# Kernel optimization log

Hardware: AMD Instinct MI355X
Metric: run time of the kernel (lower is better)

The kernel has to match this reference:

```python
import jax, jax.numpy as jnp
import numpy as np

D_MODEL = 1024
NUM_HEADS = 16
DEPTH = D_MODEL // NUM_HEADS


def setup_inputs() -> dict:
    key = jax.random.key(0)
    ks = jax.random.split(key, 11)
    B, S, D = 2, 2048, D_MODEL
    s = 1.0 / np.sqrt(D)
    inp = {
        'x': jax.random.normal(ks[0], (B, S, D), jnp.float32),
        'pH': jax.random.normal(ks[1], (B, 1, 1), jnp.float32),
        'Wq': jax.random.normal(ks[2], (D, D), jnp.float32) * s,
        'bq': jnp.zeros((D,), jnp.float32),
        'Wk': jax.random.normal(ks[3], (D, D), jnp.float32) * s,
        'bk': jnp.zeros((D,), jnp.float32),
        'Wv': jax.random.normal(ks[4], (D, D), jnp.float32) * s,
        'bv': jnp.zeros((D,), jnp.float32),
        'Wo': jax.random.normal(ks[5], (D, D), jnp.float32) * s,
        'bo': jnp.zeros((D,), jnp.float32),
    }
    return inp


def reference(x, pH, Wq, bq, Wk, bk, Wv, bv, Wo, bo):
    B, S, D = x.shape
    H, dh = NUM_HEADS, DEPTH
    # QKV projections -> [B, H, S, dh]
    def proj(W, b):
        return (x @ W + b).reshape(B, S, H, dh).transpose(0, 2, 1, 3)
    q = proj(Wq, bq)
    k = proj(Wk, bk)
    v = proj(Wv, bv)
    # scores [B, H, S, S] with additive per-sample pH bias broadcast over heads/positions
    scores = jnp.einsum('bhqd,bhkd->bhqk', q, k) / jnp.sqrt(jnp.asarray(dh, x.dtype))
    scores = scores + pH[:, :, :, None]  # [B,1,1,1] broadcasts to [B,H,S,S]
    attn = jax.nn.softmax(scores, axis=-1)
    out = jnp.einsum('bhqk,bhkd->bhqd', attn, v)  # [B,H,S,dh]
    out = out.transpose(0, 2, 1, 3).reshape(B, S, D)
    return out @ Wo + bo  # dropout p=0.0 -> identity
```

## Files before the change

### kernel.cpp

```cpp
#include <hip/hip_runtime.h>
#include <hip/hip_bf16.h>
#include <math.h>

#define BATCH 2
#define SEQ   2048
#define DMODEL 1024
#define NHEADS 16
#define DHEAD 64
#define MROWS (BATCH*SEQ)

typedef __attribute__((ext_vector_type(8))) short bf16x8;
typedef __attribute__((ext_vector_type(4))) short bf16x4;
typedef __attribute__((ext_vector_type(4))) float f32x4;

__device__ __forceinline__ short f2bf(float f) {
    union { float f; unsigned u; } c; c.f = f;
    unsigned r = (c.u + 0x7fffu + ((c.u >> 16) & 1u)) >> 16;
    return (short)r;
}
__device__ __forceinline__ float truncmask(unsigned u) {
    union { unsigned u; float f; } c; c.u = u & 0xffff0000u;
    return c.f;
}

__device__ __forceinline__ void async_ld16(const void* g, void* l) {
    __builtin_amdgcn_global_load_lds(
        (const __attribute__((address_space(1))) unsigned*)g,
        (__attribute__((address_space(3))) unsigned*)l, 16, 0, 0);
}

__global__ __launch_bounds__(256) void convert_h(
    const float* __restrict__ in, short* __restrict__ hi, int n8)
{
    const int i = blockIdx.x * 256 + threadIdx.x;
    if (i >= n8) return;
    const float4* p = (const float4*)in + (size_t)i * 2;
    float4 a = p[0], b = p[1];
    float v[8] = {a.x, a.y, a.z, a.w, b.x, b.y, b.z, b.w};
    bf16x8 H;
    #pragma unroll
    for (int j = 0; j < 8; ++j) H[j] = f2bf(v[j]);
    *((bf16x8*)hi + i) = H;
}

__global__ __launch_bounds__(256) void transpose_w4(
    const float* __restrict__ W0, const float* __restrict__ W1,
    const float* __restrict__ W2, const float* __restrict__ W3,
    short* __restrict__ oqkv, short* __restrict__ oo)
{
    __shared__ float T[64][65];
    const int tid = threadIdx.x;
    const int z = blockIdx.z;
    const float* W = (z == 0) ? W0 : (z == 1) ? W1 : (z == 2) ? W2 : W3;
    short* out = (z < 3) ? (oqkv + (size_t)z * 1024 * 1024) : oo;
    const int n0 = blockIdx.x * 64, k0 = blockIdx.y * 64;
    #pragma unroll
    for (int i = 0; i < 16; ++i) {
        const int idx = tid + i * 256;
        const int r = idx >> 6, c = idx & 63;
        T[r][c] = W[(size_t)(k0 + r) * DMODEL + n0 + c];
    }
    __syncthreads();
    #pragma unroll
    for (int i = 0; i < 4; ++i) {
        const int idx = tid + i * 256;
        const int r = idx >> 4, g = idx & 15;
        bf16x4 H;
        #pragma unroll
        for (int j = 0; j < 4; ++j)
            H[j] = f2bf(T[g * 4 + j][r]);
        *(bf16x4*)(out + (size_t)(n0 + r) * DMODEL + k0 + g * 4) = H;
    }
}

#define GBK 64

__global__ __launch_bounds__(256) void mfma_gemm(
    const short* __restrict__ Ahi, const short* __restrict__ Bthi,
    const float* __restrict__ b0, const float* __restrict__ b1, const float* __restrict__ b2,
    short* __restrict__ oqh, short* __restrict__ okh, short* __restrict__ ovh,
    float* __restrict__ outf, int mode, float qscale)
{
    __shared__ short Ah[128 * GBK], Bh[128 * GBK];

    const int tid  = threadIdx.x;
    const int lane = tid & 63;
    const int w    = tid >> 6;
    const int quad = lane >> 4;
    const int l15  = lane & 15;
    const int wr   = w >> 1, wc = w & 1;
    const int m0   = blockIdx.y * 128;
    const int n0   = blockIdx.x * 128;
    const int K    = DMODEL;

    f32x4 acc[4][4] = {};

    int srow[4], spos[4];
    #pragma unroll
    for (int j = 0; j < 4; ++j) {
        const int c = w * 256 + j * 64 + lane;
        srow[j] = c >> 3;
        spos[j] = (c & 7) ^ (srow[j] & 7);
    }

    for (int k0 = 0; k0 < K; k0 += GBK) {
        __syncthreads();
        #pragma unroll
        for (int j = 0; j < 4; ++j) {
            const int cB = (w * 256 + j * 64) * 8;
            async_ld16(Ahi + (size_t)(m0 + srow[j]) * K + k0 + spos[j] * 8, Ah + cB);
            async_ld16(Bthi + (size_t)(n0 + srow[j]) * K + k0 + spos[j] * 8, Bh + cB);
        }
        __syncthreads();

        #pragma unroll
        for (int s = 0; s < 2; ++s) {
            bf16x8 afh[4], bfh[4];
            #pragma unroll
            for (int mi = 0; mi < 4; ++mi) {
                const int row = wr * 64 + mi * 16 + l15;
                const int pos = (s * 4 + quad) ^ (row & 7);
                afh[mi] = *(const bf16x8*)(Ah + row * GBK + pos * 8);
            }
            #pragma unroll
            for (int ni = 0; ni < 4; ++ni) {
                const int row = wc * 64 + ni * 16 + l15;
                const int pos = (s * 4 + quad) ^ (row & 7);
                bfh[ni] = *(const bf16x8*)(Bh + row * GBK + pos * 8);
            }
            #pragma unroll
            for (int mi = 0; mi < 4; ++mi)
                #pragma unroll
                for (int ni = 0; ni < 4; ++ni)
                    acc[mi][ni] = __builtin_amdgcn_mfma_f32_16x16x32_bf16(
                        afh[mi], bfh[ni], acc[mi][ni], 0, 0, 0);
        }
    }

    const int nbase = n0 + wc * 64;
    if (mode == 1) {
        #pragma unroll
        for (int mi = 0; mi < 4; ++mi)
            #pragma unroll
            for (int ni = 0; ni < 4; ++ni)
                #pragma unroll
                for (int r = 0; r < 4; ++r) {
                    const int m = m0 + wr * 64 + mi * 16 + quad * 4 + r;
                    const int nn = nbase + ni * 16 + l15;
                    outf[(size_t)m * DMODEL + nn] = acc[mi][ni][r] + b0[nn];
                }
    } else {
        __syncthreads();
        short* scr = (w < 2) ? (Ah + w * 4096) : (Bh + (w - 2) * 4096);
        const int which = nbase >> 10;
        const int hh = (nbase & 1023) >> 6;
        const int mb = m0 + wr * 64;
        const int b = mb >> 11, sbase = mb & (SEQ - 1);

        if (which < 2) {
            const float* bias = which ? b1 : b0;
            short* dstp = which ? okh : oqh;
            const float scl = which ? 1.0f : qscale;
            #pragma unroll
            for (int mi = 0; mi < 4; ++mi)
                #pragma unroll
                for (int ni = 0; ni < 4; ++ni)
                    #pragma unroll
                    for (int r = 0; r < 4; ++r) {
                        const int sloc = mi * 16 + quad * 4 + r;
                        const int dloc = ni * 16 + l15;
                        const int nn = (nbase + ni * 16 + l15) & 1023;
                        scr[sloc * 64 + (((dloc >> 3) ^ (sloc & 7)) * 8) + (dloc & 7)] =
                            f2bf((acc[mi][ni][r] + bias[nn]) * scl);
                    }
            #pragma unroll
            for (int i = 0; i < 8; ++i) {
                const int sloc = i * 8 + (lane >> 3);
                const int cph = (lane & 7) ^ (sloc & 7);
                bf16x8 row = *(const bf16x8*)(scr + sloc * 64 + cph * 8);
                const int dloc = (lane & 7) * 8;
                *(bf16x8*)(dstp + ((size_t)(b * NHEADS + hh) * SEQ + sbase + sloc) * DHEAD + dloc) = row;
            }
        } else {
            #pragma unroll
            for (int mi = 0; mi < 4; ++mi)
                #pragma unroll
                for (int ni = 0; ni < 4; ++ni)
                    #pragma unroll
                    for (int r = 0; r < 4; ++r) {
                        const int sloc = mi * 16 + quad * 4 + r;
                        const int dloc = ni * 16 + l15;
                        const int nn = (nbase + ni * 16 + l15) & 1023;
                        scr[dloc * 64 + (((sloc >> 3) ^ (dloc & 7)) * 8) + (sloc & 7)] =
                            f2bf(acc[mi][ni][r] + b2[nn]);
                    }
            #pragma unroll
            for (int i = 0; i < 8; ++i) {
                const int dloc = i * 8 + (lane >> 3);
                const int cph = (lane & 7) ^ (dloc & 7);
                bf16x8 row = *(const bf16x8*)(scr + dloc * 64 + cph * 8);
                const int sg = sbase + (lane & 7) * 8;
                *(bf16x8*)(ovh + ((size_t)(b * NHEADS + hh) * DHEAD + dloc) * SEQ + sg) = row;
            }
        }
    }
}

#define PP 72

__global__ __launch_bounds__(256) void attn_mfma(
    const short* __restrict__ Qh_g, const short* __restrict__ Kh_g,
    const short* __restrict__ Vth_g, short* __restrict__ Oh_g)
{
    __shared__ short Ksh[4096];
    __shared__ short Vsh[4096];
    __shared__ short Ph[4][2][16 * PP];

    const int tid  = threadIdx.x;
    const int lane = tid & 63;
    const int w    = tid >> 6;
    const int quad = lane >> 4;
    const int l15  = lane & 15;

    const int bh    = blockIdx.x & 31;
    const int qtile = blockIdx.x >> 5;
    const int q0    = qtile * 128 + w * 32;
    const size_t kvb = (size_t)bh * SEQ * DHEAD;

    bf16x8 qA[2], qB[2];
    {
        const size_t qrA = kvb + (size_t)(q0 + l15) * DHEAD;
        const size_t qrB = kvb + (size_t)(q0 + 16 + l15) * DHEAD;
        qA[0] = *(const bf16x8*)(Qh_g + qrA + quad * 8);
        qA[1] = *(const bf16x8*)(Qh_g + qrA + 32 + quad * 8);
        qB[0] = *(const bf16x8*)(Qh_g + qrB + quad * 8);
        qB[1] = *(const bf16x8*)(Qh_g + qrB + 32 + quad * 8);
    }

    short* dst = (w < 2) ? Ksh : Vsh;
    const bool isv = (w >= 2);
    int srow[4], spos[4];
    #pragma unroll
    for (int j = 0; j < 4; ++j) {
        const int c = (w & 1) * 256 + j * 64 + lane;
        srow[j] = c >> 3;
        spos[j] = (c & 7) ^ (srow[j] & 7);
    }

    f32x4 oA[4] = {}, oB[4] = {};
    float lA = 0.f, lB = 0.f;

    for (int kb = 0; kb < SEQ; kb += 64) {
        __syncthreads();
        {
            const short* src = isv ? (Vth_g + kvb + kb) : (Kh_g + kvb + (size_t)kb * DHEAD);
            #pragma unroll
            for (int j = 0; j < 4; ++j) {
                const short* g = src + (isv ? ((size_t)srow[j] * SEQ + spos[j] * 8)
                                            : ((size_t)srow[j] * DHEAD + spos[j] * 8));
                async_ld16(g, dst + ((w & 1) * 256 + j * 64) * 8);
            }
        }
        __syncthreads();

        #pragma unroll
        for (int mf = 0; mf < 4; ++mf) {
            const int row = mf * 16 + l15;
            const int sw = row & 7;
            bf16x8 kh0 = *(const bf16x8*)(Ksh + row * 64 + ((quad ^ sw) * 8));
            bf16x8 kh1 = *(const bf16x8*)(Ksh + row * 64 + (((4 + quad) ^ sw) * 8));
            f32x4 cA = {}, cB = {};
            cA = __builtin_amdgcn_mfma_f32_16x16x32_bf16(kh0, qA[0], cA, 0, 0, 0);
            cA = __builtin_amdgcn_mfma_f32_16x16x32_bf16(kh1, qA[1], cA, 0, 0, 0);
            cB = __builtin_amdgcn_mfma_f32_16x16x32_bf16(kh0, qB[0], cB, 0, 0, 0);
            cB = __builtin_amdgcn_mfma_f32_16x16x32_bf16(kh1, qB[1], cB, 0, 0, 0);

            unsigned uA[4], uB[4];
            #pragma unroll
            for (int r = 0; r < 4; ++r) {
                union { float f; unsigned u; } p;
                p.f = __builtin_amdgcn_exp2f(cA[r]);
                uA[r] = p.u; lA += truncmask(uA[r]);
                p.f = __builtin_amdgcn_exp2f(cB[r]);
                uB[r] = p.u; lB += truncmask(uB[r]);
            }
            uint2 pkA, pkB;
            pkA.x = __builtin_amdgcn_perm(uA[1], uA[0], 0x07060302u);
            pkA.y = __builtin_amdgcn_perm(uA[3], uA[2], 0x07060302u);
            pkB.x = __builtin_amdgcn_perm(uB[1], uB[0], 0x07060302u);
            pkB.y = __builtin_amdgcn_perm(uB[3], uB[2], 0x07060302u);
            *(uint2*)(&Ph[w][0][l15 * PP + mf * 16 + quad * 4]) = pkA;
            *(uint2*)(&Ph[w][1][l15 * PP + mf * 16 + quad * 4]) = pkB;
        }

        bf16x8 pA0 = *(const bf16x8*)(&Ph[w][0][l15 * PP + quad * 8]);
        bf16x8 pA1 = *(const bf16x8*)(&Ph[w][0][l15 * PP + 32 + quad * 8]);
        bf16x8 pB0 = *(const bf16x8*)(&Ph[w][1][l15 * PP + quad * 8]);
        bf16x8 pB1 = *(const bf16x8*)(&Ph[w][1][l15 * PP + 32 + quad * 8]);

        #pragma unroll
        for (int nf = 0; nf < 4; ++nf) {
            const int row = nf * 16 + l15;
            const int sw = row & 7;
            bf16x8 vh0 = *(const bf16x8*)(Vsh + row * 64 + ((quad ^ sw) * 8));
            bf16x8 vh1 = *(const bf16x8*)(Vsh + row * 64 + (((4 + quad) ^ sw) * 8));
            f32x4 cA = oA[nf], cB = oB[nf];
            cA = __builtin_amdgcn_mfma_f32_16x16x32_bf16(pA0, vh0, cA, 0, 0, 0);
            cA = __builtin_amdgcn_mfma_f32_16x16x32_bf16(pA1, vh1, cA, 0, 0, 0);
            cB = __builtin_amdgcn_mfma_f32_16x16x32_bf16(pB0, vh0, cB, 0, 0, 0);
            cB = __builtin_amdgcn_mfma_f32_16x16x32_bf16(pB1, vh1, cB, 0, 0, 0);
            oA[nf] = cA; oB[nf] = cB;
        }
    }

    float lsA = lA, lsB = lB;
    lsA += __shfl_xor(lsA, 16, 64);  lsA += __shfl_xor(lsA, 32, 64);
    lsB += __shfl_xor(lsB, 16, 64);  lsB += __shfl_xor(lsB, 32, 64);
    float liA[4], liB[4];
    #pragma unroll
    for (int r = 0; r < 4; ++r) {
        liA[r] = 1.0f / __shfl(lsA, quad * 4 + r, 64);
        liB[r] = 1.0f / __shfl(lsB, quad * 4 + r, 64);
    }

    const int b = bh >> 4, hh = bh & 15;
    #pragma unroll
    for (int nf = 0; nf < 4; ++nf) {
        #pragma unroll
        for (int r = 0; r < 4; ++r) {
            const int qa = q0 + quad * 4 + r;
            const int d = nf * 16 + l15;
            Oh_g[(size_t)(b * SEQ + qa) * DMODEL + hh * DHEAD + d] = f2bf(oA[nf][r] * liA[r]);
            Oh_g[(size_t)(b * SEQ + qa + 16) * DMODEL + hh * DHEAD + d] = f2bf(oB[nf][r] * liB[r]);
        }
    }
}

extern "C" void kernel_launch(void* const* d_in, const int* in_sizes, int n_in,
                              void* d_out, int out_size, void* d_ws, size_t ws_size,
                              hipStream_t stream) {
    const float* x  = (const float*)d_in[0];
    const float* Wq = (const float*)d_in[2];
    const float* bq = (const float*)d_in[3];
    const float* Wk = (const float*)d_in[4];
    const float* bk = (const float*)d_in[5];
    const float* Wv = (const float*)d_in[6];
    const float* bv = (const float*)d_in[7];
    const float* Wo = (const float*)d_in[8];
    const float* bo = (const float*)d_in[9];
    float* out = (float*)d_out;

    char* ws = (char*)d_ws;
    const size_t MB = 1024 * 1024;
    short* qh  = (short*)(ws + 0 * MB);
    short* kh  = (short*)(ws + 16 * MB);
    short* vth = (short*)(ws + 32 * MB);
    short* aoh = (short*)(ws + 48 * MB);
    short* xhi = (short*)(ws + 64 * MB);
    short* wqkv_hi = (short*)(ws + 80 * MB);
    short* wto_hi  = (short*)(ws + 92 * MB);

    dim3 blk(256);
    const int n8 = MROWS * DMODEL / 8;

    hipLaunchKernelGGL(convert_h, dim3(n8 / 256), blk, 0, stream, x, xhi, n8);
    hipLaunchKernelGGL(transpose_w4, dim3(16, 16, 4), blk, 0, stream,
                       Wq, Wk, Wv, Wo, wqkv_hi, wto_hi);

    const float qscale = 0.125f * 1.44269504088896f;
    hipLaunchKernelGGL(mfma_gemm, dim3(3072 / 128, MROWS / 128), blk, 0, stream,
                       xhi, wqkv_hi, bq, bk, bv,
                       qh, kh, vth, (float*)nullptr, 0, qscale);

    hipLaunchKernelGGL(attn_mfma, dim3(BATCH * NHEADS * (SEQ / 128)), blk, 0, stream,
                       qh, kh, vth, aoh);

    hipLaunchKernelGGL(mfma_gemm, dim3(1024 / 128, MROWS / 128), blk, 0, stream,
                       aoh, wto_hi, bo, bo, bo,
                       (short*)nullptr, (short*)nullptr, (short*)nullptr,
                       out, 1, 1.0f);
}
```

Measured before the change: 210.4 us.

## Double-buffer K/V tiles in LDS and compute softmax row sums via MFMA

The attention kernel now keeps two LDS buffers for K and V. It issues the async global-to-LDS load for the next 64-key block before computing on the current one, so each iteration needs one barrier instead of two and load latency overlaps with MFMA work. Softmax denominators are now accumulated with extra MFMAs against a vector of bf16 ones, reusing the P fragments. This replaces the per-element VALU adds and the cross-lane shuffle reduction. The cost is double the K/V shared memory, which may lower occupancy, plus four extra MFMAs per key block.

```diff
diff --git a/kernel.cpp b/kernel.cpp
--- a/kernel.cpp
+++ b/kernel.cpp
@@ -17,10 +17,6 @@
     union { float f; unsigned u; } c; c.f = f;
     unsigned r = (c.u + 0x7fffu + ((c.u >> 16) & 1u)) >> 16;
     return (short)r;
-}
-__device__ __forceinline__ float truncmask(unsigned u) {
-    union { unsigned u; float f; } c; c.u = u & 0xffff0000u;
-    return c.f;
 }
 
 __device__ __forceinline__ void async_ld16(const void* g, void* l) {
@@ -212,8 +208,8 @@
     const short* __restrict__ Qh_g, const short* __restrict__ Kh_g,
     const short* __restrict__ Vth_g, short* __restrict__ Oh_g)
 {
-    __shared__ short Ksh[4096];
-    __shared__ short Vsh[4096];
+    __shared__ short Ksh[2][4096];
+    __shared__ short Vsh[2][4096];
     __shared__ short Ph[4][2][16 * PP];
 
     const int tid  = threadIdx.x;
@@ -226,6 +222,10 @@
     const int qtile = blockIdx.x >> 5;
     const int q0    = qtile * 128 + w * 32;
     const size_t kvb = (size_t)bh * SEQ * DHEAD;
+
+    bf16x8 ones;
+    #pragma unroll
+    for (int j = 0; j < 8; ++j) ones[j] = (short)0x3f80;
 
     bf16x8 qA[2], qB[2];
     {
@@ -237,7 +237,6 @@
         qB[1] = *(const bf16x8*)(Qh_g + qrB + 32 + quad * 8);
     }
 
-    short* dst = (w < 2) ? Ksh : Vsh;
     const bool isv = (w >= 2);
     int srow[4], spos[4];
     #pragma unroll
@@ -247,28 +246,35 @@
         spos[j] = (c & 7) ^ (srow[j] & 7);
     }
 
+    auto stage = [&](int buf, int kb) {
+        short* d = isv ? Vsh[buf] : Ksh[buf];
+        const short* src = isv ? (Vth_g + kvb + kb) : (Kh_g + kvb + (size_t)kb * DHEAD);
+        #pragma unroll
+        for (int j = 0; j < 4; ++j) {
+            const short* g = src + (isv ? ((size_t)srow[j] * SEQ + spos[j] * 8)
+                                        : ((size_t)srow[j] * DHEAD + spos[j] * 8));
+            async_ld16(g, d + ((w & 1) * 256 + j * 64) * 8);
+        }
+    };
+
     f32x4 oA[4] = {}, oB[4] = {};
-    float lA = 0.f, lB = 0.f;
-
-    for (int kb = 0; kb < SEQ; kb += 64) {
+    f32x4 lAv = {}, lBv = {};
+
+    stage(0, 0);
+    int pb = 0;
+    for (int kb = 0; kb < SEQ; kb += 64, pb ^= 1) {
         __syncthreads();
-        {
-            const short* src = isv ? (Vth_g + kvb + kb) : (Kh_g + kvb + (size_t)kb * DHEAD);
-            #pragma unroll
-            for (int j = 0; j < 4; ++j) {
-                const short* g = src + (isv ? ((size_t)srow[j] * SEQ + spos[j] * 8)
-                                            : ((size_t)srow[j] * DHEAD + spos[j] * 8));
-                async_ld16(g, dst + ((w & 1) * 256 + j * 64) * 8);
-            }
-        }
-        __syncthreads();
+        if (kb + 64 < SEQ) stage(pb ^ 1, kb + 64);
+
+        const short* Kb = Ksh[pb];
+        const short* Vb = Vsh[pb];
 
         #pragma unroll
         for (int mf = 0; mf < 4; ++mf) {
             const int row = mf * 16 + l15;
             const int sw = row & 7;
-            bf16x8 kh0 = *(const bf16x8*)(Ksh + row * 64 + ((quad ^ sw) * 8));
-            bf16x8 kh1 = *(const bf16x8*)(Ksh + row * 64 + (((4 + quad) ^ sw) * 8));
+            bf16x8 kh0 = *(const bf16x8*)(Kb + row * 64 + ((quad ^ sw) * 8));
+            bf16x8 kh1 = *(const bf16x8*)(Kb + row * 64 + (((4 + quad) ^ sw) * 8));
             f32x4 cA = {}, cB = {};
             cA = __builtin_amdgcn_mfma_f32_16x16x32_bf16(kh0, qA[0], cA, 0, 0, 0);
             cA = __builtin_amdgcn_mfma_f32_16x16x32_bf16(kh1, qA[1], cA, 0, 0, 0);
@@ -280,9 +286,9 @@
             for (int r = 0; r < 4; ++r) {
                 union { float f; unsigned u; } p;
                 p.f = __builtin_amdgcn_exp2f(cA[r]);
-                uA[r] = p.u; lA += truncmask(uA[r]);
+                uA[r] = p.u;
                 p.f = __builtin_amdgcn_exp2f(cB[r]);
-                uB[r] = p.u; lB += truncmask(uB[r]);
+                uB[r] = p.u;
             }
             uint2 pkA, pkB;
             pkA.x = __builtin_amdgcn_perm(uA[1], uA[0], 0x07060302u);
@@ -298,12 +304,17 @@
         bf16x8 pB0 = *(const bf16x8*)(&Ph[w][1][l15 * PP + quad * 8]);
         bf16x8 pB1 = *(const bf16x8*)(&Ph[w][1][l15 * PP + 32 + quad * 8]);
 
+        lAv = __builtin_amdgcn_mfma_f32_16x16x32_bf16(pA0, ones, lAv, 0, 0, 0);
+        lAv = __builtin_amdgcn_mfma_f32_16x16x32_bf16(pA1, ones, lAv, 0, 0, 0);
+        lBv = __builtin_amdgcn_mfma_f32_16x16x32_bf16(pB0, ones, lBv, 0, 0, 0);
+        lBv = __builtin_amdgcn_mfma_f32_16x16x32_bf16(pB1, ones, lBv, 0, 0, 0);
+
         #pragma unroll
         for (int nf = 0; nf < 4; ++nf) {
             const int row = nf * 16 + l15;
             const int sw = row & 7;
-            bf16x8 vh0 = *(const bf16x8*)(Vsh + row * 64 + ((quad ^ sw) * 8));
-            bf16x8 vh1 = *(const bf16x8*)(Vsh + row * 64 + (((4 + quad) ^ sw) * 8));
+            bf16x8 vh0 = *(const bf16x8*)(Vb + row * 64 + ((quad ^ sw) * 8));
+            bf16x8 vh1 = *(const bf16x8*)(Vb + row * 64 + (((4 + quad) ^ sw) * 8));
             f32x4 cA = oA[nf], cB = oB[nf];
             cA = __builtin_amdgcn_mfma_f32_16x16x32_bf16(pA0, vh0, cA, 0, 0, 0);
             cA = __builtin_amdgcn_mfma_f32_16x16x32_bf16(pA1, vh1, cA, 0, 0, 0);
@@ -313,14 +324,11 @@
         }
     }
 
-    float lsA = lA, lsB = lB;
-    lsA += __shfl_xor(lsA, 16, 64);  lsA += __shfl_xor(lsA, 32, 64);
-    lsB += __shfl_xor(lsB, 16, 64);  lsB += __shfl_xor(lsB, 32, 64);
     float liA[4], liB[4];
     #pragma unroll
     for (int r = 0; r < 4; ++r) {
-        liA[r] = 1.0f / __shfl(lsA, quad * 4 + r, 64);
-        liB[r] = 1.0f / __shfl(lsB, quad * 4 + r, 64);
+        liA[r] = 1.0f / lAv[r];
+        liB[r] = 1.0f / lBv[r];
     }
 
     const int b = bh >> 4, hh = bh & 15;
```

Result: no change. 208.8 us (-0.7%).
